# Performance work log

Hardware: AMD Instinct MI355X
Metric: run time of the kernel (lower is better)

## Reference

```python
import jax, jax.numpy as jnp
import numpy as np

B, N, G, K = 4, 2048, 8, 16
C_IN = K * 3 + 3  # in_features_size=0 path: conv1 in = 0 + local_n*3 + 3 = 51
CH = [C_IN, 32, 48, 64, 80, 96]  # feature_size(4i, 4i*3) = 16i for i=2..6
THR = 0.1  # weight_threshold


def setup_inputs() -> dict:
    key = jax.random.key(0)
    ks = jax.random.split(key, 3 + 3 * 5)
    inp = {
        "point_cloud": jax.random.normal(ks[0], (B, N, 3), jnp.float32),
        "normals": jax.random.normal(ks[1], (B, N, 3), jnp.float32),
        "dr_w": jax.random.uniform(ks[2], (B, N, G), jnp.float32),
    }
    for i in range(5):
        cin, cout = CH[i], CH[i + 1]
        k0 = 3 + 3 * i
        inp[f"W{i+1}"] = jax.random.normal(ks[k0], (cin, cout), jnp.float32) * (1.0 / np.sqrt(cin))
        inp[f"b{i+1}"] = jnp.zeros((cout,), jnp.float32)
        inp[f"s{i+1}"] = 1.0 + 0.1 * jax.random.normal(ks[k0 + 1], (cout,), jnp.float32)  # BN (eval) scale
        inp[f"o{i+1}"] = 0.01 * jax.random.normal(ks[k0 + 2], (cout,), jnp.float32)      # BN (eval) shift
    return inp


def _forward(point_cloud, normals, dr_w, params):
    # sign-flip group for full (non rotation-only) 3D frames: 8 ops, flips eigenvector columns
    OPS = jnp.array([[1, 1, 1], [1, 1, -1], [1, -1, 1], [1, -1, -1],
                     [-1, 1, 1], [-1, 1, -1], [-1, -1, 1], [-1, -1, -1]], jnp.float32)
    wn = jnp.swapaxes(dr_w, 1, 2)                                  # [B,G,N]
    wsum = dr_w.sum(1)                                             # [B,G]
    wnorm = dr_w / (dr_w.sum(1, keepdims=True) + 1e-6)             # [B,N,G]
    # --- get_frame (weighted): weighted center + weighted covariance + eigh per group ---
    center = jnp.einsum('bnd,bng->bgd', point_cloud, wnorm)        # [B,G,3]
    pc = point_cloud[:, None, :, :] - center[:, :, None, :]        # [B,G,N,3]
    Rm = jnp.einsum('bgnd,bgn,bgne->bgde', pc, wn, pc)             # [B,G,3,3]
    deg = (wsum > 1.0).astype(Rm.dtype)[..., None, None]           # degenerate-group guard
    noise = jax.random.normal(jax.random.key(42), Rm.shape, Rm.dtype)
    lambdas, V = jnp.linalg.eigh(deg * Rm + (1.0 - deg) * noise)
    frames = jax.lax.stop_gradient(V)                              # is_detach_frame=True
    center = jax.lax.stop_gradient(center)
    F_ops = OPS[None, :, None, None, :] * frames[:, None]          # [B,8,G,3,3]
    # --- soft-weighted kNN over points ---
    ww = jnp.einsum('bng,bmg->bnm', dr_w, dr_w)                    # [B,N,N]
    sq = jnp.sum((point_cloud[:, :, None, :] - point_cloud[:, None, :, :]) ** 2, -1)
    d = ww * sq + (1.0 - ww) * 1000.0
    _, idx = jax.lax.top_k(-d, K)                                  # smallest K -> [B,N,K]
    pnts_n = jax.vmap(lambda p, i: p[i])(point_cloud, idx)         # [B,N,K,3]
    # v1 = (1-w)*center + w*pnts_n - center = w*(pnts_n - center)
    v1 = wn[..., None, None] * (pnts_n[:, None] - center[:, :, None, None, :])  # [B,G,N,K,3]
    # v2: weighted normals blended with per-group weighted mean normal
    nw = normals[:, None, :, :] * wn[..., None]                    # [B,G,N,3]
    nmean = nw.sum(2) / (wsum[..., None] + 1e-6)                   # [B,G,3]
    v2 = nw + (1.0 - wn)[..., None] * nmean[:, :, None, :]         # [B,G,N,3]
    # apply equivariant frames: (F_ops^T @ v^T)^T == v @ F_ops
    f1 = jnp.einsum('bgnkd,bogde->bognke', v1, F_ops)              # [B,8,G,N,K,3]
    f2 = jnp.einsum('bgnd,bogde->bogne', v2, F_ops)                # [B,8,G,N,3]
    x = jnp.concatenate([f1.reshape(B, 8, G, N, K * 3), f2], -1)   # [B,8,G,N,51]
    # MinkowskiLinear + BN(eval affine) + ReLU stack, applied densely then masked
    for (W, b, s, o) in params:
        x = jax.nn.relu((x @ W + b) * s + o)
    mask = (wn >= THR).astype(x.dtype)[:, None, :, :, None]        # weight_threshold filter
    return x * mask                                                # [B,8,G,N,96]


def reference(point_cloud, normals, dr_w,
              W1, b1, s1, o1, W2, b2, s2, o2, W3, b3, s3, o3,
              W4, b4, s4, o4, W5, b5, s5, o5):
    params = [(W1, b1, s1, o1), (W2, b2, s2, o2), (W3, b3, s3, o3),
              (W4, b4, s4, o4), (W5, b5, s5, o5)]
    return _forward(point_cloud, normals, dr_w, params)
```

## Files before the change

### kernel.cpp

```cpp
#include <hip/hip_runtime.h>
#include <math.h>

#define NPTS 2048
#define BATCH 4
#define NG 8
#define KNN_K 16
#define FR_OFF 512
#define IDX_OFF 1024
#define WOFF_F (IDX_OFF + BATCH * NPTS * KNN_K)
#define FLOATMAX 3.402823466e38f

typedef __attribute__((ext_vector_type(8))) short bf16x8;
typedef __attribute__((ext_vector_type(4))) float f32x4;

__device__ inline unsigned short bf16_rne(float x) {
  unsigned u = __float_as_uint(x);
  u += 0x7FFFu + ((u >> 16) & 1u);
  return (unsigned short)(u >> 16);
}
__device__ inline float bf16_f(unsigned short h) {
  return __uint_as_float(((unsigned)h) << 16);
}

__global__ void stats_kernel(const float* __restrict__ pc, const float* __restrict__ nrm,
                             const float* __restrict__ drw, float* __restrict__ ws) {
  __shared__ float red[256];
  int bg = blockIdx.x;
  int b = bg >> 3, g = bg & 7;
  int t = threadIdx.x;

  float sw = 0.f, sp0 = 0.f, sp1 = 0.f, sp2 = 0.f, sn0 = 0.f, sn1 = 0.f, sn2 = 0.f;
  for (int n = t; n < NPTS; n += 256) {
    float w = drw[((size_t)b * NPTS + n) * NG + g];
    const float* p = pc + ((size_t)b * NPTS + n) * 3;
    const float* nr = nrm + ((size_t)b * NPTS + n) * 3;
    sw += w;
    sp0 += w * p[0]; sp1 += w * p[1]; sp2 += w * p[2];
    sn0 += w * nr[0]; sn1 += w * nr[1]; sn2 += w * nr[2];
  }

  auto blockReduce = [&](float v) -> float {
    red[t] = v; __syncthreads();
    for (int s = 128; s > 0; s >>= 1) {
      if (t < s) red[t] += red[t + s];
      __syncthreads();
    }
    float r = red[0];
    __syncthreads();
    return r;
  };

  float Sw = blockReduce(sw);
  float inv = 1.f / (Sw + 1e-6f);
  float C0 = blockReduce(sp0) * inv;
  float C1 = blockReduce(sp1) * inv;
  float C2 = blockReduce(sp2) * inv;
  float M0 = blockReduce(sn0) * inv;
  float M1 = blockReduce(sn1) * inv;
  float M2 = blockReduce(sn2) * inv;

  float r00 = 0.f, r10 = 0.f, r11 = 0.f, r20 = 0.f, r21 = 0.f, r22 = 0.f;
  for (int n = t; n < NPTS; n += 256) {
    float w = drw[((size_t)b * NPTS + n) * NG + g];
    const float* p = pc + ((size_t)b * NPTS + n) * 3;
    float p0 = p[0] - C0, p1 = p[1] - C1, p2 = p[2] - C2;
    r00 += w * p0 * p0;
    r10 += w * p1 * p0;
    r11 += w * p1 * p1;
    r20 += w * p2 * p0;
    r21 += w * p2 * p1;
    r22 += w * p2 * p2;
  }
  float R00 = blockReduce(r00);
  float R10 = blockReduce(r10);
  float R11 = blockReduce(r11);
  float R20 = blockReduce(r20);
  float R21 = blockReduce(r21);
  float R22 = blockReduce(r22);

  if (t == 0) {
    float* st = ws + bg * 16;
    st[0] = Sw;
    st[1] = C0; st[2] = C1; st[3] = C2;
    st[4] = M0; st[5] = M1; st[6] = M2;
    st[7] = R00; st[8] = R10; st[9] = R11; st[10] = R20; st[11] = R21; st[12] = R22;
  }
}

__device__ inline float slapy2f(float x, float y) {
  float ax = fabsf(x), ay = fabsf(y);
  float w = fmaxf(ax, ay), z = fminf(ax, ay);
  if (z == 0.f) return w;
  float q = z / w;
  return w * sqrtf(1.f + q * q);
}

__device__ inline void slartgf(float f, float g, float& c, float& s, float& r) {
  if (g == 0.f) { c = 1.f; s = 0.f; r = f; }
  else if (f == 0.f) { c = 0.f; s = (g >= 0.f) ? 1.f : -1.f; r = fabsf(g); }
  else {
    float d = sqrtf(f * f + g * g);
    c = fabsf(f) / d;
    r = (f >= 0.f) ? d : -d;
    s = g / r;
  }
}

__device__ void slaev2f(float a, float b, float c, float& rt1, float& rt2, float& cs1, float& sn1) {
  float sm = a + c, df = a - c, adf = fabsf(df), tb = b + b, ab = fabsf(tb);
  float acmx, acmn;
  if (fabsf(a) > fabsf(c)) { acmx = a; acmn = c; } else { acmx = c; acmn = a; }
  float rt;
  if (adf > ab) { float t = ab / adf; rt = adf * sqrtf(1.f + t * t); }
  else if (adf < ab) { float t = adf / ab; rt = ab * sqrtf(1.f + t * t); }
  else rt = ab * sqrtf(2.f);
  int sgn1;
  if (sm < 0.f) { rt1 = 0.5f * (sm - rt); sgn1 = -1; rt2 = (acmx / rt1) * acmn - (b / rt1) * b; }
  else if (sm > 0.f) { rt1 = 0.5f * (sm + rt); sgn1 = 1; rt2 = (acmx / rt1) * acmn - (b / rt1) * b; }
  else { rt1 = 0.5f * rt; rt2 = -0.5f * rt; sgn1 = 1; }
  float cs; int sgn2;
  if (df >= 0.f) { cs = df + rt; sgn2 = 1; } else { cs = df - rt; sgn2 = -1; }
  float acs = fabsf(cs);
  if (acs > ab) {
    float ct = -tb / cs;
    sn1 = 1.f / sqrtf(1.f + ct * ct);
    cs1 = ct * sn1;
  } else {
    if (ab == 0.f) { cs1 = 1.f; sn1 = 0.f; }
    else {
      float tn = -cs / tb;
      cs1 = 1.f / sqrtf(1.f + tn * tn);
      sn1 = tn * cs1;
    }
  }
  if (sgn1 == sgn2) { float tn = cs1; cs1 = -sn1; sn1 = tn; }
}

__device__ void steqr3(float d[3], float e[2], float Z[3][3]) {
  const float eps = 5.9604645e-08f;
  const float eps2 = eps * eps;
  const float safmin = 1.17549435e-38f;
  const int nmaxit = 90;
  const int n = 3;
  int jtot = 0;
  int l1 = 0;
  while (l1 <= n - 1) {
    if (l1 > 0) e[l1 - 1] = 0.f;
    int m;
    for (m = l1; m <= n - 2; m++) {
      float tst = fabsf(e[m]);
      if (tst == 0.f) break;
      if (tst <= (sqrtf(fabsf(d[m])) * sqrtf(fabsf(d[m + 1]))) * eps) { e[m] = 0.f; break; }
    }
    int l = l1, lend = m;
    l1 = m + 1;
    if (lend == l) continue;
    if (fabsf(d[lend]) < fabsf(d[l])) { int tmp = l; l = lend; lend = tmp; }
    if (lend > l) {
      for (;;) {
        int mm = lend;
        if (l != lend) {
          for (mm = l; mm <= lend - 1; mm++) {
            float tst = e[mm] * e[mm];
            if (tst <= eps2 * fabsf(d[mm]) * fabsf(d[mm + 1]) + safmin) break;
          }
        }
        if (mm < lend) e[mm] = 0.f;
        float p = d[l];
        if (mm == l) {
          d[l] = p; l++;
          if (l <= lend) continue; else break;
        }
        if (mm == l + 1) {
          float rt1, rt2, c, s;
          slaev2f(d[l], e[l], d[l + 1], rt1, rt2, c, s);
          #pragma unroll
          for (int i = 0; i < 3; i++) {
            float tp = Z[i][l + 1];
            Z[i][l + 1] = c * tp - s * Z[i][l];
            Z[i][l] = s * tp + c * Z[i][l];
          }
          d[l] = rt1; d[l + 1] = rt2; e[l] = 0.f;
          l += 2;
          if (l <= lend) continue; else break;
        }
        if (jtot == nmaxit) break;
        jtot++;
        float g = (d[l + 1] - p) / (2.f * e[l]);
        float r = slapy2f(g, 1.f);
        g = d[mm] - p + e[l] / (g + copysignf(r, g));
        float s = 1.f, c = 1.f;
        p = 0.f;
        float cs[2], sn[2];
        for (int i = mm - 1; i >= l; i--) {
          float f = s * e[i];
          float bb = c * e[i];
          slartgf(g, f, c, s, r);
          if (i != mm - 1) e[i + 1] = r;
          g = d[i + 1] - p;
          r = (d[i] - g) * s + 2.f * c * bb;
          p = s * r;
          d[i + 1] = g + p;
          g = c * r - bb;
          cs[i] = c; sn[i] = -s;
        }
        for (int jj = mm - l - 1; jj >= 0; jj--) {
          float c_ = cs[l + jj], s_ = sn[l + jj];
          #pragma unroll
          for (int i = 0; i < 3; i++) {
            float tp = Z[i][l + jj + 1];
            Z[i][l + jj + 1] = c_ * tp - s_ * Z[i][l + jj];
            Z[i][l + jj] = s_ * tp + c_ * Z[i][l + jj];
          }
        }
        d[l] -= p;
        e[l] = g;
      }
    } else {
      for (;;) {
        int mm = lend;
        if (l != lend) {
          for (mm = l; mm >= lend + 1; mm--) {
            float tst = e[mm - 1] * e[mm - 1];
            if (tst <= eps2 * fabsf(d[mm]) * fabsf(d[mm - 1]) + safmin) break;
          }
        }
        if (mm > lend) e[mm - 1] = 0.f;
        float p = d[l];
        if (mm == l) {
          d[l] = p; l--;
          if (l >= lend) continue; else break;
        }
        if (mm == l - 1) {
          float rt1, rt2, c, s;
          slaev2f(d[l - 1], e[l - 1], d[l], rt1, rt2, c, s);
          #pragma unroll
          for (int i = 0; i < 3; i++) {
            float tp = Z[i][l];
            Z[i][l] = c * tp - s * Z[i][l - 1];
            Z[i][l - 1] = s * tp + c * Z[i][l - 1];
          }
          d[l - 1] = rt1; d[l] = rt2; e[l - 1] = 0.f;
          l -= 2;
          if (l >= lend) continue; else break;
        }
        if (jtot == nmaxit) break;
        jtot++;
        float g = (d[l - 1] - p) / (2.f * e[l - 1]);
        float r = slapy2f(g, 1.f);
        g = d[mm] - p + e[l - 1] / (g + copysignf(r, g));
        float s = 1.f, c = 1.f;
        p = 0.f;
        float cs[2], sn[2];
        for (int i = mm; i <= l - 1; i++) {
          float f = s * e[i];
          float bb = c * e[i];
          slartgf(g, f, c, s, r);
          if (i != mm) e[i - 1] = r;
          g = d[i] - p;
          r = (d[i + 1] - g) * s + 2.f * c * bb;
          p = s * r;
          d[i] = g + p;
          g = c * r - bb;
          cs[i] = c; sn[i] = s;
        }
        for (int jj = 0; jj <= l - mm - 1; jj++) {
          float c_ = cs[mm + jj], s_ = sn[mm + jj];
          #pragma unroll
          for (int i = 0; i < 3; i++) {
            float tp = Z[i][mm + jj + 1];
            Z[i][mm + jj + 1] = c_ * tp - s_ * Z[i][mm + jj];
            Z[i][mm + jj] = s_ * tp + c_ * Z[i][mm + jj];
          }
        }
        d[l] -= p;
        e[l - 1] = g;
      }
    }
  }
  for (int ii = 1; ii < 3; ii++) {
    int i = ii - 1, k = i;
    float p = d[i];
    for (int j = ii; j < 3; j++) if (d[j] < p) { k = j; p = d[j]; }
    if (k != i) {
      d[k] = d[i]; d[i] = p;
      for (int r2 = 0; r2 < 3; r2++) {
        float tp = Z[r2][i]; Z[r2][i] = Z[r2][k]; Z[r2][k] = tp;
      }
    }
  }
}

__global__ void eigh_kernel(float* __restrict__ ws) {
  if (threadIdx.x != 0) return;
  int id = blockIdx.x;
  const float* st = ws + id * 16;
  float A00 = st[7], A10 = st[8], A11 = st[9], A20 = st[10], A21 = st[11], A22 = st[12];

  float d[3], e[2];
  float tau = 0.f, u2 = 0.f;
  d[0] = A00;
  float alpha = A10, x31 = A20;
  if (x31 == 0.f) {
    tau = 0.f; u2 = 0.f;
    d[1] = A11; d[2] = A22; e[0] = alpha; e[1] = A21;
  } else {
    float nrm = slapy2f(alpha, fabsf(x31));
    float beta = (alpha >= 0.f) ? -nrm : nrm;
    tau = (beta - alpha) / beta;
    u2 = (1.f / (alpha - beta)) * x31;
    float x1 = tau * (A11 + A21 * u2);
    float x2 = tau * (A21 + A22 * u2);
    float al = -0.5f * tau * (x1 + x2 * u2);
    x1 = x1 + al;
    x2 = x2 + al * u2;
    d[1] = A11 - 2.f * x1;
    e[1] = A21 - (u2 * x1 + x2);
    d[2] = A22 - 2.f * (u2 * x2);
    e[0] = beta;
  }

  float Z[3][3] = {{1.f, 0.f, 0.f}, {0.f, 1.f, 0.f}, {0.f, 0.f, 1.f}};
  steqr3(d, e, Z);

  if (tau != 0.f) {
    for (int j = 0; j < 3; j++) {
      float w = Z[1][j] + u2 * Z[2][j];
      float tw = tau * w;
      Z[1][j] -= tw;
      Z[2][j] -= tw * u2;
    }
  }
  float* fr = ws + FR_OFF + id * 9;
  for (int dd = 0; dd < 3; dd++)
    for (int ee = 0; ee < 3; ee++)
      fr[dd * 3 + ee] = Z[dd][ee];
}

__global__ __launch_bounds__(256, 4) void knn_kernel(const float* __restrict__ pc,
                                                     const float* __restrict__ drw,
                                                     int* __restrict__ idxout) {
  int t = threadIdx.x;
  int lane = t & 63;
  int q = blockIdx.x * 4 + (t >> 6);
  int b = q >> 11;
  int n = q & (NPTS - 1);

  const float* qp = pc + ((size_t)b * NPTS + n) * 3;
  float q0 = qp[0], q1 = qp[1], q2 = qp[2];
  const float4* qw4 = (const float4*)(drw + ((size_t)b * NPTS + n) * NG);
  float4 qa = qw4[0], qb = qw4[1];

  float d[32];
  #pragma unroll
  for (int j = 0; j < 32; j++) {
    int m = j * 64 + lane;
    const float4* mw4 = (const float4*)(drw + ((size_t)b * NPTS + m) * NG);
    float4 ma = mw4[0], mb = mw4[1];
    float ww = qa.x * ma.x + qa.y * ma.y + qa.z * ma.z + qa.w * ma.w
             + qb.x * mb.x + qb.y * mb.y + qb.z * mb.z + qb.w * mb.w;
    const float* mp = pc + ((size_t)b * NPTS + m) * 3;
    float dx = q0 - mp[0], dy = q1 - mp[1], dz = q2 - mp[2];
    float sq = dx * dx + dy * dy + dz * dz;
    d[j] = ww * sq + (1.f - ww) * 1000.f;
    if ((j & 3) == 3) __builtin_amdgcn_sched_barrier(0);
  }

  int myres = 0;
  #pragma unroll 1
  for (int r = 0; r < KNN_K; r++) {
    float bd = d[0];
    int bj = 0;
    #pragma unroll
    for (int j = 1; j < 32; j++) {
      if (d[j] < bd) { bd = d[j]; bj = j; }
    }
    int gm = bj * 64 + lane;
    #pragma unroll
    for (int s = 1; s < 64; s <<= 1) {
      float od = __shfl_xor(bd, s, 64);
      int om = __shfl_xor(gm, s, 64);
      if (od < bd || (od == bd && om < gm)) { bd = od; gm = om; }
    }
    if (lane == r) myres = gm;
    int ls = gm & 63, js = gm >> 6;
    if (lane == ls) {
      #pragma unroll
      for (int j = 0; j < 32; j++) {
        if (j == js) d[j] = FLOATMAX;
      }
    }
  }
  if (lane < KNN_K) idxout[(size_t)q * KNN_K + lane] = myres;
}

__global__ void wprep_kernel(const float* __restrict__ W1, const float* __restrict__ W2,
                             const float* __restrict__ W3, const float* __restrict__ W4,
                             const float* __restrict__ W5, float* __restrict__ ws) {
  const int FB[5] = {0, 4, 7, 15, 25};
  const int NTs[5] = {2, 3, 4, 5, 6};
  const int CINs[5] = {51, 32, 48, 64, 80};
  const int COUTs[5] = {32, 48, 64, 80, 96};
  const float* Ws[5] = {W1, W2, W3, W4, W5};

  int fp = blockIdx.x;
  int layer = 0;
  while (layer < 4 && fp >= FB[layer + 1]) layer++;
  int rel = fp - FB[layer];
  int kt = rel / NTs[layer], nt = rel % NTs[layer];
  int lane = threadIdx.x;
  int c = nt * 16 + (lane & 15);
  int q = lane >> 4;
  int cin = CINs[layer], cout = COUTs[layer];
  const float* W = Ws[layer];

  unsigned short* wb = (unsigned short*)(ws + WOFF_F);
  unsigned short* dH = wb + fp * 1024 + lane * 8;
  unsigned short* dL = dH + 512;
  for (int i = 0; i < 8; i++) {
    int k = kt * 32 + q * 8 + i;
    float w = (k < cin) ? W[(size_t)k * cout + c] : 0.f;
    unsigned short hb = bf16_rne(w);
    dH[i] = hb;
    dL[i] = bf16_rne(w - bf16_f(hb));
  }
}

#define ASTRIDE 104

template <int CIN, int COUT, int FB>
__device__ inline void mfma_layer(const unsigned short* __restrict__ wfr,
                                  const unsigned short* inH, const unsigned short* inL,
                                  unsigned short* outH, unsigned short* outL,
                                  const float* __restrict__ Bb, const float* __restrict__ Ss,
                                  const float* __restrict__ Oo, int lane, int wv) {
  constexpr int KT = (CIN + 31) / 32;
  constexpr int NT = COUT / 16;
  int r = lane & 15, q = lane >> 4;
  int arow = (wv * 16 + r) * ASTRIDE;

  f32x4 acc[NT];
  #pragma unroll
  for (int i = 0; i < NT; i++) acc[i] = (f32x4){0.f, 0.f, 0.f, 0.f};

  #pragma unroll
  for (int kt = 0; kt < KT; kt++) {
    bf16x8 ah = *(const bf16x8*)(inH + arow + kt * 32 + q * 8);
    bf16x8 al = *(const bf16x8*)(inL + arow + kt * 32 + q * 8);
    #pragma unroll
    for (int nt = 0; nt < NT; nt++) {
      int fid = FB + kt * NT + nt;
      bf16x8 bh = *(const bf16x8*)(wfr + fid * 1024 + lane * 8);
      bf16x8 bl = *(const bf16x8*)(wfr + fid * 1024 + 512 + lane * 8);
      acc[nt] = __builtin_amdgcn_mfma_f32_16x16x32_bf16(ah, bh, acc[nt], 0, 0, 0);
      acc[nt] = __builtin_amdgcn_mfma_f32_16x16x32_bf16(ah, bl, acc[nt], 0, 0, 0);
      acc[nt] = __builtin_amdgcn_mfma_f32_16x16x32_bf16(al, bh, acc[nt], 0, 0, 0);
    }
  }

  #pragma unroll
  for (int nt = 0; nt < NT; nt++) {
    int c = nt * 16 + r;
    float bb = Bb[c], ss = Ss[c], oo = Oo[c];
    #pragma unroll
    for (int j = 0; j < 4; j++) {
      float h = fmaxf(fmaf(acc[nt][j] + bb, ss, oo), 0.f);
      unsigned short hb = bf16_rne(h);
      int rr = (wv * 16 + q * 4 + j) * ASTRIDE + c;
      outH[rr] = hb;
      outL[rr] = bf16_rne(h - bf16_f(hb));
    }
  }
}

__global__ __launch_bounds__(256) void mlp_kernel(
    const float* __restrict__ pc, const float* __restrict__ nrm, const float* __restrict__ drw,
    const int* __restrict__ kidx, const float* __restrict__ ws,
    const float* __restrict__ B1, const float* __restrict__ S1, const float* __restrict__ O1,
    const float* __restrict__ B2, const float* __restrict__ S2, const float* __restrict__ O2,
    const float* __restrict__ B3, const float* __restrict__ S3, const float* __restrict__ O3,
    const float* __restrict__ B4, const float* __restrict__ S4, const float* __restrict__ O4,
    const float* __restrict__ B5, const float* __restrict__ S5, const float* __restrict__ O5,
    float* __restrict__ out) {
  __shared__ __align__(16) unsigned short actH[2][64 * ASTRIDE];
  __shared__ __align__(16) unsigned short actL[2][64 * ASTRIDE];
  __shared__ float sfr[9], sc[3], snm[3], swn[8];

  int t = threadIdx.x;
  int bi = blockIdx.x;
  int b = bi >> 11;
  int g = (bi >> 8) & 7;
  int n0 = (bi & 255) << 3;
  int bg = b * 8 + g;

  if (t < 9) sfr[t] = ws[FR_OFF + bg * 9 + t];
  else if (t >= 16 && t < 19) sc[t - 16] = ws[bg * 16 + 1 + (t - 16)];
  else if (t >= 32 && t < 35) snm[t - 32] = ws[bg * 16 + 4 + (t - 32)];
  else if (t >= 64 && t < 72) swn[t - 64] = drw[((size_t)b * NPTS + n0 + (t - 64)) * NG + g];

  {
    unsigned* zH = (unsigned*)actH;
    unsigned* zL = (unsigned*)actL;
    #pragma unroll
    for (int z = 0; z < 26; z++) {
      zH[z * 256 + t] = 0u;
      zL[z * 256 + t] = 0u;
    }
  }
  __syncthreads();

  if (t < 128) {
    int i = t >> 4, kk = t & 15;
    int n = n0 + i;
    int id = kidx[((size_t)b * NPTS + n) * KNN_K + kk];
    const float* p = pc + ((size_t)b * NPTS + id) * 3;
    float w = swn[i];
    float v0 = w * (p[0] - sc[0]);
    float v1 = w * (p[1] - sc[1]);
    float v2 = w * (p[2] - sc[2]);
    #pragma unroll
    for (int e = 0; e < 3; e++) {
      float gv = v0 * sfr[e] + v1 * sfr[3 + e] + v2 * sfr[6 + e];
      unsigned short hb = bf16_rne(gv);
      unsigned short lb = bf16_rne(gv - bf16_f(hb));
      int f = 3 * kk + e;
      #pragma unroll
      for (int op = 0; op < 8; op++) {
        int sb = (e == 0) ? (op >> 2) : (e == 1) ? (op >> 1) : op;
        unsigned short sgn = (unsigned short)((sb & 1) << 15);
        int rr = (i * 8 + op) * ASTRIDE + f;
        actH[0][rr] = (unsigned short)(hb ^ sgn);
        actL[0][rr] = (unsigned short)(lb ^ sgn);
      }
    }
  } else if (t < 136) {
    int i = t - 128;
    int n = n0 + i;
    float w = swn[i];
    const float* nr = nrm + ((size_t)b * NPTS + n) * 3;
    float v0 = nr[0] * w + (1.f - w) * snm[0];
    float v1 = nr[1] * w + (1.f - w) * snm[1];
    float v2 = nr[2] * w + (1.f - w) * snm[2];
    #pragma unroll
    for (int e = 0; e < 3; e++) {
      float gv = v0 * sfr[e] + v1 * sfr[3 + e] + v2 * sfr[6 + e];
      unsigned short hb = bf16_rne(gv);
      unsigned short lb = bf16_rne(gv - bf16_f(hb));
      int f = 48 + e;
      #pragma unroll
      for (int op = 0; op < 8; op++) {
        int sb = (e == 0) ? (op >> 2) : (e == 1) ? (op >> 1) : op;
        unsigned short sgn = (unsigned short)((sb & 1) << 15);
        int rr = (i * 8 + op) * ASTRIDE + f;
        actH[0][rr] = (unsigned short)(hb ^ sgn);
        actL[0][rr] = (unsigned short)(lb ^ sgn);
      }
    }
  }
  __syncthreads();

  const unsigned short* wfr = (const unsigned short*)(ws + WOFF_F);
  int lane = t & 63;
  int wv = t >> 6;

  mfma_layer<51, 32, 0>(wfr, actH[0], actL[0], actH[1], actL[1], B1, S1, O1, lane, wv);
  __syncthreads();
  mfma_layer<32, 48, 4>(wfr, actH[1], actL[1], actH[0], actL[0], B2, S2, O2, lane, wv);
  __syncthreads();
  mfma_layer<48, 64, 7>(wfr, actH[0], actL[0], actH[1], actL[1], B3, S3, O3, lane, wv);
  __syncthreads();
  mfma_layer<64, 80, 15>(wfr, actH[1], actL[1], actH[0], actL[0], B4, S4, O4, lane, wv);
  __syncthreads();

  {
    constexpr int KT = 3, NT = 6, FB = 25;
    int r = lane & 15, q = lane >> 4;
    int arow = (wv * 16 + r) * ASTRIDE;
    f32x4 acc[NT];
    #pragma unroll
    for (int i = 0; i < NT; i++) acc[i] = (f32x4){0.f, 0.f, 0.f, 0.f};
    #pragma unroll
    for (int kt = 0; kt < KT; kt++) {
      bf16x8 ah = *(const bf16x8*)(actH[0] + arow + kt * 32 + q * 8);
      bf16x8 al = *(const bf16x8*)(actL[0] + arow + kt * 32 + q * 8);
      #pragma unroll
      for (int nt = 0; nt < NT; nt++) {
        int fid = FB + kt * NT + nt;
        bf16x8 bh = *(const bf16x8*)(wfr + fid * 1024 + lane * 8);
        bf16x8 bl = *(const bf16x8*)(wfr + fid * 1024 + 512 + lane * 8);
        acc[nt] = __builtin_amdgcn_mfma_f32_16x16x32_bf16(ah, bh, acc[nt], 0, 0, 0);
        acc[nt] = __builtin_amdgcn_mfma_f32_16x16x32_bf16(ah, bl, acc[nt], 0, 0, 0);
        acc[nt] = __builtin_amdgcn_mfma_f32_16x16x32_bf16(al, bh, acc[nt], 0, 0, 0);
      }
    }
    #pragma unroll
    for (int nt = 0; nt < NT; nt++) {
      int c = nt * 16 + r;
      float bb = B5[c], ss = S5[c], oo = O5[c];
      #pragma unroll
      for (int j = 0; j < 4; j++) {
        int rr = wv * 16 + q * 4 + j;
        int i = rr >> 3, op = rr & 7;
        int n = n0 + i;
        float h = fmaxf(fmaf(acc[nt][j] + bb, ss, oo), 0.f);
        float hv = (swn[i] >= 0.1f) ? h : 0.f;
        out[((((size_t)(b * 8 + op)) * NG + g) * NPTS + n) * 96 + c] = hv;
      }
    }
  }
}

extern "C" void kernel_launch(void* const* d_in, const int* in_sizes, int n_in,
                              void* d_out, int out_size, void* d_ws, size_t ws_size,
                              hipStream_t stream) {
  const float* pc = (const float*)d_in[0];
  const float* nrm = (const float*)d_in[1];
  const float* drw = (const float*)d_in[2];
  const float* W1 = (const float*)d_in[3];
  const float* B1 = (const float*)d_in[4];
  const float* S1 = (const float*)d_in[5];
  const float* O1 = (const float*)d_in[6];
  const float* W2 = (const float*)d_in[7];
  const float* B2 = (const float*)d_in[8];
  const float* S2 = (const float*)d_in[9];
  const float* O2 = (const float*)d_in[10];
  const float* W3 = (const float*)d_in[11];
  const float* B3 = (const float*)d_in[12];
  const float* S3 = (const float*)d_in[13];
  const float* O3 = (const float*)d_in[14];
  const float* W4 = (const float*)d_in[15];
  const float* B4 = (const float*)d_in[16];
  const float* S4 = (const float*)d_in[17];
  const float* O4 = (const float*)d_in[18];
  const float* W5 = (const float*)d_in[19];
  const float* B5 = (const float*)d_in[20];
  const float* S5 = (const float*)d_in[21];
  const float* O5 = (const float*)d_in[22];
  float* out = (float*)d_out;
  float* wsf = (float*)d_ws;
  int* idxw = (int*)(wsf + IDX_OFF);

  wprep_kernel<<<43, 64, 0, stream>>>(W1, W2, W3, W4, W5, wsf);
  stats_kernel<<<32, 256, 0, stream>>>(pc, nrm, drw, wsf);
  eigh_kernel<<<32, 64, 0, stream>>>(wsf);
  knn_kernel<<<BATCH * NPTS / 4, 256, 0, stream>>>(pc, drw, idxw);
  mlp_kernel<<<BATCH * NG * (NPTS / 8), 256, 0, stream>>>(
      pc, nrm, drw, idxw, wsf,
      B1, S1, O1, B2, S2, O2, B3, S3, O3,
      B4, S4, O4, B5, S5, O5, out);
}
```

Measured before the change: 446.3 us.

## Merge prep kernels, drop inter-layer barriers and shrink MLP LDS footprint

Folds the stats and weight-prep kernels into one launch, and folds the eigensolver blocks into the KNN launch, cutting the launch count from five to three. In the MLP kernel it removes the block barriers between layers, which is valid because each wave reads and writes only its own 16 activation rows. It also replaces the uniform 104-element row stride with alternating 88/72 strides to cut shared memory and allow more resident blocks. Per-group scalars are now read from global memory instead of staged in shared memory, which trades a little extra global traffic for fewer shared stores and one less barrier dependency.

```diff
diff --git a/kernel.cpp b/kernel.cpp
--- a/kernel.cpp
+++ b/kernel.cpp
@@ -20,71 +20,6 @@
 }
 __device__ inline float bf16_f(unsigned short h) {
   return __uint_as_float(((unsigned)h) << 16);
-}
-
-__global__ void stats_kernel(const float* __restrict__ pc, const float* __restrict__ nrm,
-                             const float* __restrict__ drw, float* __restrict__ ws) {
-  __shared__ float red[256];
-  int bg = blockIdx.x;
-  int b = bg >> 3, g = bg & 7;
-  int t = threadIdx.x;
-
-  float sw = 0.f, sp0 = 0.f, sp1 = 0.f, sp2 = 0.f, sn0 = 0.f, sn1 = 0.f, sn2 = 0.f;
-  for (int n = t; n < NPTS; n += 256) {
-    float w = drw[((size_t)b * NPTS + n) * NG + g];
-    const float* p = pc + ((size_t)b * NPTS + n) * 3;
-    const float* nr = nrm + ((size_t)b * NPTS + n) * 3;
-    sw += w;
-    sp0 += w * p[0]; sp1 += w * p[1]; sp2 += w * p[2];
-    sn0 += w * nr[0]; sn1 += w * nr[1]; sn2 += w * nr[2];
-  }
-
-  auto blockReduce = [&](float v) -> float {
-    red[t] = v; __syncthreads();
-    for (int s = 128; s > 0; s >>= 1) {
-      if (t < s) red[t] += red[t + s];
-      __syncthreads();
-    }
-    float r = red[0];
-    __syncthreads();
-    return r;
-  };
-
-  float Sw = blockReduce(sw);
-  float inv = 1.f / (Sw + 1e-6f);
-  float C0 = blockReduce(sp0) * inv;
-  float C1 = blockReduce(sp1) * inv;
-  float C2 = blockReduce(sp2) * inv;
-  float M0 = blockReduce(sn0) * inv;
-  float M1 = blockReduce(sn1) * inv;
-  float M2 = blockReduce(sn2) * inv;
-
-  float r00 = 0.f, r10 = 0.f, r11 = 0.f, r20 = 0.f, r21 = 0.f, r22 = 0.f;
-  for (int n = t; n < NPTS; n += 256) {
-    float w = drw[((size_t)b * NPTS + n) * NG + g];
-    const float* p = pc + ((size_t)b * NPTS + n) * 3;
-    float p0 = p[0] - C0, p1 = p[1] - C1, p2 = p[2] - C2;
-    r00 += w * p0 * p0;
-    r10 += w * p1 * p0;
-    r11 += w * p1 * p1;
-    r20 += w * p2 * p0;
-    r21 += w * p2 * p1;
-    r22 += w * p2 * p2;
-  }
-  float R00 = blockReduce(r00);
-  float R10 = blockReduce(r10);
-  float R11 = blockReduce(r11);
-  float R20 = blockReduce(r20);
-  float R21 = blockReduce(r21);
-  float R22 = blockReduce(r22);
-
-  if (t == 0) {
-    float* st = ws + bg * 16;
-    st[0] = Sw;
-    st[1] = C0; st[2] = C1; st[3] = C2;
-    st[4] = M0; st[5] = M1; st[6] = M2;
-    st[7] = R00; st[8] = R10; st[9] = R11; st[10] = R20; st[11] = R21; st[12] = R22;
-  }
 }
 
 __device__ inline float slapy2f(float x, float y) {
@@ -291,9 +226,7 @@
   }
 }
 
-__global__ void eigh_kernel(float* __restrict__ ws) {
-  if (threadIdx.x != 0) return;
-  int id = blockIdx.x;
+__device__ void eigh_one(float* __restrict__ ws, int id) {
   const float* st = ws + id * 16;
   float A00 = st[7], A10 = st[8], A11 = st[9], A20 = st[10], A21 = st[11], A22 = st[12];
 
@@ -337,12 +270,118 @@
       fr[dd * 3 + ee] = Z[dd][ee];
 }
 
-__global__ __launch_bounds__(256, 4) void knn_kernel(const float* __restrict__ pc,
-                                                     const float* __restrict__ drw,
-                                                     int* __restrict__ idxout) {
+__global__ void prep_kernel(const float* __restrict__ pc, const float* __restrict__ nrm,
+                            const float* __restrict__ drw,
+                            const float* __restrict__ W1, const float* __restrict__ W2,
+                            const float* __restrict__ W3, const float* __restrict__ W4,
+                            const float* __restrict__ W5, float* __restrict__ ws) {
+  __shared__ float red[256];
+  int t = threadIdx.x;
+
+  if (blockIdx.x < 32) {
+    int bg = blockIdx.x;
+    int b = bg >> 3, g = bg & 7;
+
+    float sw = 0.f, sp0 = 0.f, sp1 = 0.f, sp2 = 0.f, sn0 = 0.f, sn1 = 0.f, sn2 = 0.f;
+    for (int n = t; n < NPTS; n += 256) {
+      float w = drw[((size_t)b * NPTS + n) * NG + g];
+      const float* p = pc + ((size_t)b * NPTS + n) * 3;
+      const float* nr = nrm + ((size_t)b * NPTS + n) * 3;
+      sw += w;
+      sp0 += w * p[0]; sp1 += w * p[1]; sp2 += w * p[2];
+      sn0 += w * nr[0]; sn1 += w * nr[1]; sn2 += w * nr[2];
+    }
+
+    auto blockReduce = [&](float v) -> float {
+      red[t] = v; __syncthreads();
+      for (int s = 128; s > 0; s >>= 1) {
+        if (t < s) red[t] += red[t + s];
+        __syncthreads();
+      }
+      float r = red[0];
+      __syncthreads();
+      return r;
+    };
+
+    float Sw = blockReduce(sw);
+    float inv = 1.f / (Sw + 1e-6f);
+    float C0 = blockReduce(sp0) * inv;
+    float C1 = blockReduce(sp1) * inv;
+    float C2 = blockReduce(sp2) * inv;
+    float M0 = blockReduce(sn0) * inv;
+    float M1 = blockReduce(sn1) * inv;
+    float M2 = blockReduce(sn2) * inv;
+
+    float r00 = 0.f, r10 = 0.f, r11 = 0.f, r20 = 0.f, r21 = 0.f, r22 = 0.f;
+    for (int n = t; n < NPTS; n += 256) {
+      float w = drw[((size_t)b * NPTS + n) * NG + g];
+      const float* p = pc + ((size_t)b * NPTS + n) * 3;
+      float p0 = p[0] - C0, p1 = p[1] - C1, p2 = p[2] - C2;
+      r00 += w * p0 * p0;
+      r10 += w * p1 * p0;
+      r11 += w * p1 * p1;
+      r20 += w * p2 * p0;
+      r21 += w * p2 * p1;
+      r22 += w * p2 * p2;
+    }
+    float R00 = blockReduce(r00);
+    float R10 = blockReduce(r10);
+    float R11 = blockReduce(r11);
+    float R20 = blockReduce(r20);
+    float R21 = blockReduce(r21);
+    float R22 = blockReduce(r22);
+
+    if (t == 0) {
+      float* st = ws + bg * 16;
+      st[0] = Sw;
+      st[1] = C0; st[2] = C1; st[3] = C2;
+      st[4] = M0; st[5] = M1; st[6] = M2;
+      st[7] = R00; st[8] = R10; st[9] = R11; st[10] = R20; st[11] = R21; st[12] = R22;
+    }
+    return;
+  }
+
+  if (t >= 64) return;
+  const int FB[5] = {0, 4, 7, 15, 25};
+  const int NTs[5] = {2, 3, 4, 5, 6};
+  const int CINs[5] = {51, 32, 48, 64, 80};
+  const int COUTs[5] = {32, 48, 64, 80, 96};
+  const float* Ws[5] = {W1, W2, W3, W4, W5};
+
+  int fp = blockIdx.x - 32;
+  int layer = 0;
+  while (layer < 4 && fp >= FB[layer + 1]) layer++;
+  int rel = fp - FB[layer];
+  int kt = rel / NTs[layer], nt = rel % NTs[layer];
+  int lane = t;
+  int c = nt * 16 + (lane & 15);
+  int q = lane >> 4;
+  int cin = CINs[layer], cout = COUTs[layer];
+  const float* W = Ws[layer];
+
+  unsigned short* wb = (unsigned short*)(ws + WOFF_F);
+  unsigned short* dH = wb + fp * 1024 + lane * 8;
+  unsigned short* dL = dH + 512;
+  for (int i = 0; i < 8; i++) {
+    int k = kt * 32 + q * 8 + i;
+    float w = (k < cin) ? W[(size_t)k * cout + c] : 0.f;
+    unsigned short hb = bf16_rne(w);
+    dH[i] = hb;
+    dL[i] = bf16_rne(w - bf16_f(hb));
+  }
+}
+
+__global__ __launch_bounds__(256, 4) void knn_eigh_kernel(const float* __restrict__ pc,
+                                                          const float* __restrict__ drw,
+                                                          int* __restrict__ idxout,
+                                                          float* __restrict__ ws) {
+  if (blockIdx.x < 32) {
+    if (threadIdx.x == 0) eigh_one(ws, blockIdx.x);
+    return;
+  }
   int t = threadIdx.x;
   int lane = t & 63;
-  int q = blockIdx.x * 4 + (t >> 6);
+  int q = (blockIdx.x - 32) * 4 + (t >> 6);
   int b = q >> 11;
   int n = q & (NPTS - 1);
 
@@ -394,41 +433,10 @@
   if (lane < KNN_K) idxout[(size_t)q * KNN_K + lane] = myres;
 }
 
-__global__ void wprep_kernel(const float* __restrict__ W1, const float* __restrict__ W2,
-                             const float* __restrict__ W3, const float* __restrict__ W4,
-                             const float* __restrict__ W5, float* __restrict__ ws) {
-  const int FB[5] = {0, 4, 7, 15, 25};
-  const int NTs[5] = {2, 3, 4, 5, 6};
-  const int CINs[5] = {51, 32, 48, 64, 80};
-  const int COUTs[5] = {32, 48, 64, 80, 96};
-  const float* Ws[5] = {W1, W2, W3, W4, W5};
-
-  int fp = blockIdx.x;
-  int layer = 0;
-  while (layer < 4 && fp >= FB[layer + 1]) layer++;
-  int rel = fp - FB[layer];
-  int kt = rel / NTs[layer], nt = rel % NTs[layer];
-  int lane = threadIdx.x;
-  int c = nt * 16 + (lane & 15);
-  int q = lane >> 4;
-  int cin = CINs[layer], cout = COUTs[layer];
-  const float* W = Ws[layer];
-
-  unsigned short* wb = (unsigned short*)(ws + WOFF_F);
-  unsigned short* dH = wb + fp * 1024 + lane * 8;
-  unsigned short* dL = dH + 512;
-  for (int i = 0; i < 8; i++) {
-    int k = kt * 32 + q * 8 + i;
-    float w = (k < cin) ? W[(size_t)k * cout + c] : 0.f;
-    unsigned short hb = bf16_rne(w);
-    dH[i] = hb;
-    dL[i] = bf16_rne(w - bf16_f(hb));
-  }
-}
-
-#define ASTRIDE 104
-
-template <int CIN, int COUT, int FB>
+#define SB0 88
+#define SB1 72
+
+template <int CIN, int COUT, int FB, int SIN, int SOUT>
 __device__ inline void mfma_layer(const unsigned short* __restrict__ wfr,
                                   const unsigned short* inH, const unsigned short* inL,
                                   unsigned short* outH, unsigned short* outL,
@@ -437,7 +445,7 @@
   constexpr int KT = (CIN + 31) / 32;
   constexpr int NT = COUT / 16;
   int r = lane & 15, q = lane >> 4;
-  int arow = (wv * 16 + r) * ASTRIDE;
+  int arow = (wv * 16 + r) * SIN;
 
   f32x4 acc[NT];
   #pragma unroll
@@ -466,7 +474,7 @@
     for (int j = 0; j < 4; j++) {
       float h = fmaxf(fmaf(acc[nt][j] + bb, ss, oo), 0.f);
       unsigned short hb = bf16_rne(h);
-      int rr = (wv * 16 + q * 4 + j) * ASTRIDE + c;
+      int rr = (wv * 16 + q * 4 + j) * SOUT + c;
       outH[rr] = hb;
       outL[rr] = bf16_rne(h - bf16_f(hb));
     }
@@ -482,9 +490,11 @@
     const float* __restrict__ B4, const float* __restrict__ S4, const float* __restrict__ O4,
     const float* __restrict__ B5, const float* __restrict__ S5, const float* __restrict__ O5,
     float* __restrict__ out) {
-  __shared__ __align__(16) unsigned short actH[2][64 * ASTRIDE];
-  __shared__ __align__(16) unsigned short actL[2][64 * ASTRIDE];
-  __shared__ float sfr[9], sc[3], snm[3], swn[8];
+  __shared__ __align__(16) unsigned short smem[20480];
+  unsigned short* aH0 = smem;
+  unsigned short* aH1 = smem + 5632;
+  unsigned short* aL0 = smem + 10240;
+  unsigned short* aL1 = smem + 15872;
 
   int t = threadIdx.x;
   int bi = blockIdx.x;
@@ -493,19 +503,10 @@
   int n0 = (bi & 255) << 3;
   int bg = b * 8 + g;
 
-  if (t < 9) sfr[t] = ws[FR_OFF + bg * 9 + t];
-  else if (t >= 16 && t < 19) sc[t - 16] = ws[bg * 16 + 1 + (t - 16)];
-  else if (t >= 32 && t < 35) snm[t - 32] = ws[bg * 16 + 4 + (t - 32)];
-  else if (t >= 64 && t < 72) swn[t - 64] = drw[((size_t)b * NPTS + n0 + (t - 64)) * NG + g];
-
   {
-    unsigned* zH = (unsigned*)actH;
-    unsigned* zL = (unsigned*)actL;
-    #pragma unroll
-    for (int z = 0; z < 26; z++) {
-      zH[z * 256 + t] = 0u;
-      zL[z * 256 + t] = 0u;
-    }
+    unsigned* z = (unsigned*)smem;
+    #pragma unroll
+    for (int zz = 0; zz < 40; zz++) z[zz * 256 + t] = 0u;
   }
   __syncthreads();
 
@@ -514,13 +515,15 @@
     int n = n0 + i;
     int id = kidx[((size_t)b * NPTS + n) * KNN_K + kk];
     const float* p = pc + ((size_t)b * NPTS + id) * 3;
-    float w = swn[i];
-    float v0 = w * (p[0] - sc[0]);
-    float v1 = w * (p[1] - sc[1]);
-    float v2 = w * (p[2] - sc[2]);
+    const float* fr = ws + FR_OFF + bg * 9;
+    const float* ct = ws + bg * 16 + 1;
+    float w = drw[((size_t)b * NPTS + n) * NG + g];
+    float v0 = w * (p[0] - ct[0]);
+    float v1 = w * (p[1] - ct[1]);
+    float v2 = w * (p[2] - ct[2]);
     #pragma unroll
     for (int e = 0; e < 3; e++) {
-      float gv = v0 * sfr[e] + v1 * sfr[3 + e] + v2 * sfr[6 + e];
+      float gv = v0 * fr[e] + v1 * fr[3 + e] + v2 * fr[6 + e];
       unsigned short hb = bf16_rne(gv);
       unsigned short lb = bf16_rne(gv - bf16_f(hb));
       int f = 3 * kk + e;
@@ -528,22 +531,24 @@
       for (int op = 0; op < 8; op++) {
         int sb = (e == 0) ? (op >> 2) : (e == 1) ? (op >> 1) : op;
         unsigned short sgn = (unsigned short)((sb & 1) << 15);
-        int rr = (i * 8 + op) * ASTRIDE + f;
-        actH[0][rr] = (unsigned short)(hb ^ sgn);
-        actL[0][rr] = (unsigned short)(lb ^ sgn);
+        int rr = (i * 8 + op) * SB0 + f;
+        aH0[rr] = (unsigned short)(hb ^ sgn);
+        aL0[rr] = (unsigned short)(lb ^ sgn);
       }
     }
   } else if (t < 136) {
     int i = t - 128;
     int n = n0 + i;
-    float w = swn[i];
+    float w = drw[((size_t)b * NPTS + n) * NG + g];
     const float* nr = nrm + ((size_t)b * NPTS + n) * 3;
-    float v0 = nr[0] * w + (1.f - w) * snm[0];
-    float v1 = nr[1] * w + (1.f - w) * snm[1];
-    float v2 = nr[2] * w + (1.f - w) * snm[2];
+    const float* fr = ws + FR_OFF + bg * 9;
+    const float* nm = ws + bg * 16 + 4;
+    float v0 = nr[0] * w + (1.f - w) * nm[0];
+    float v1 = nr[1] * w + (1.f - w) * nm[1];
+    float v2 = nr[2] * w + (1.f - w) * nm[2];
     #pragma unroll
     for (int e = 0; e < 3; e++) {
-      float gv = v0 * sfr[e] + v1 * sfr[3 + e] + v2 * sfr[6 + e];
+      float gv = v0 * fr[e] + v1 * fr[3 + e] + v2 * fr[6 + e];
       unsigned short hb = bf16_rne(gv);
       unsigned short lb = bf16_rne(gv - bf16_f(hb));
       int f = 48 + e;
@@ -551,9 +556,9 @@
       for (int op = 0; op < 8; op++) {
         int sb = (e == 0) ? (op >> 2) : (e == 1) ? (op >> 1) : op;
         unsigned short sgn = (unsigned short)((sb & 1) << 15);
-        int rr = (i * 8 + op) * ASTRIDE + f;
-        actH[0][rr] = (unsigned short)(hb ^ sgn);
-        actL[0][rr] = (unsigned short)(lb ^ sgn);
+        int rr = (i * 8 + op) * SB0 + f;
+        aH0[rr] = (unsigned short)(hb ^ sgn);
+        aL0[rr] = (unsigned short)(lb ^ sgn);
       }
     }
   }
@@ -563,26 +568,22 @@
   int lane = t & 63;
   int wv = t >> 6;
 
-  mfma_layer<51, 32, 0>(wfr, actH[0], actL[0], actH[1], actL[1], B1, S1, O1, lane, wv);
-  __syncthreads();
-  mfma_layer<32, 48, 4>(wfr, actH[1], actL[1], actH[0], actL[0], B2, S2, O2, lane, wv);
-  __syncthreads();
-  mfma_layer<48, 64, 7>(wfr, actH[0], actL[0], actH[1], actL[1], B3, S3, O3, lane, wv);
-  __syncthreads();
-  mfma_layer<64, 80, 15>(wfr, actH[1], actL[1], actH[0], actL[0], B4, S4, O4, lane, wv);
-  __syncthreads();
+  mfma_layer<51, 32, 0, SB0, SB1>(wfr, aH0, aL0, aH1, aL1, B1, S1, O1, lane, wv);
+  mfma_layer<32, 48, 4, SB1, SB0>(wfr, aH1, aL1, aH0, aL0, B2, S2, O2, lane, wv);
+  mfma_layer<48, 64, 7, SB0, SB1>(wfr, aH0, aL0, aH1, aL1, B3, S3, O3, lane, wv);
+  mfma_layer<64, 80, 15, SB1, SB0>(wfr, aH1, aL1, aH0, aL0, B4, S4, O4, lane, wv);
 
   {
     constexpr int KT = 3, NT = 6, FB = 25;
     int r = lane & 15, q = lane >> 4;
-    int arow = (wv * 16 + r) * ASTRIDE;
+    int arow = (wv * 16 + r) * SB0;
     f32x4 acc[NT];
     #pragma unroll
     for (int i = 0; i < NT; i++) acc[i] = (f32x4){0.f, 0.f, 0.f, 0.f};
     #pragma unroll
     for (int kt = 0; kt < KT; kt++) {
-      bf16x8 ah = *(const bf16x8*)(actH[0] + arow + kt * 32 + q * 8);
-      bf16x8 al = *(const bf16x8*)(actL[0] + arow + kt * 32 + q * 8);
+      bf16x8 ah = *(const bf16x8*)(aH0 + arow + kt * 32 + q * 8);
+      bf16x8 al = *(const bf16x8*)(aL0 + arow + kt * 32 + q * 8);
       #pragma unroll
       for (int nt = 0; nt < NT; nt++) {
         int fid = FB + kt * NT + nt;
@@ -593,18 +594,20 @@
         acc[nt] = __builtin_amdgcn_mfma_f32_16x16x32_bf16(al, bh, acc[nt], 0, 0, 0);
       }
     }
+    int i = 2 * wv + (q >> 1);
+    int n = n0 + i;
+    float wlane = drw[((size_t)b * NPTS + n) * NG + g];
+    float maskv = (wlane >= 0.1f) ? 1.f : 0.f;
+    int opbase = (q & 1) * 4;
     #pragma unroll
     for (int nt = 0; nt < NT; nt++) {
       int c = nt * 16 + r;
       float bb = B5[c], ss = S5[c], oo = O5[c];
       #pragma unroll
       for (int j = 0; j < 4; j++) {
-        int rr = wv * 16 + q * 4 + j;
-        int i = rr >> 3, op = rr & 7;
-        int n = n0 + i;
+        int op = opbase + j;
         float h = fmaxf(fmaf(acc[nt][j] + bb, ss, oo), 0.f);
-        float hv = (swn[i] >= 0.1f) ? h : 0.f;
-        out[((((size_t)(b * 8 + op)) * NG + g) * NPTS + n) * 96 + c] = hv;
+        out[((((size_t)(b * 8 + op)) * NG + g) * NPTS + n) * 96 + c] = h * maskv;
       }
     }
   }
@@ -640,10 +643,8 @@
   float* wsf = (float*)d_ws;
   int* idxw = (int*)(wsf + IDX_OFF);
 
-  wprep_kernel<<<43, 64, 0, stream>>>(W1, W2, W3, W4, W5, wsf);
-  stats_kernel<<<32, 256, 0, stream>>>(pc, nrm, drw, wsf);
-  eigh_kernel<<<32, 64, 0, stream>>>(wsf);
-  knn_kernel<<<BATCH * NPTS / 4, 256, 0, stream>>>(pc, drw, idxw);
+  prep_kernel<<<75, 256, 0, stream>>>(pc, nrm, drw, W1, W2, W3, W4, W5, wsf);
+  knn_eigh_kernel<<<32 + BATCH * NPTS / 4, 256, 0, stream>>>(pc, drw, idxw, wsf);
   mlp_kernel<<<BATCH * NG * (NPTS / 8), 256, 0, stream>>>(
       pc, nrm, drw, idxw, wsf,
       B1, S1, O1, B2, S2, O2, B3, S3, O3,
```

After: 389.1 us. 12.8% less time.
